# Kernel tuning notes

Hardware: AMD Instinct MI355X
Metric: run time of the kernel (lower is better)

The kernel has to match this reference:

```python
import jax, jax.numpy as jnp
import numpy as np

BITS = 4
N_PACK = 8  # 32-bit container / 4-bit values
GROUPSIZE = 128
MASK = (1 << BITS) - 1


def _unpack(packed, n_valid):
    # packed: [R, ceil(n_valid/N_PACK)] int32 -> [R, n_valid] int32 nibbles
    shifts = (jnp.arange(N_PACK, dtype=jnp.int32) * BITS)
    vals = (packed[:, :, None] >> shifts) & MASK  # [R, C, N_PACK]
    return vals.reshape(packed.shape[0], -1)[:, :n_valid]


def setup_inputs() -> dict:
    key = jax.random.key(0)
    k0, k1, k2, k3, k4 = jax.random.split(key, 5)
    O, I = 4096, 4096
    ng = I // GROUPSIZE  # 32
    x = jax.random.normal(k0, (2, 2048, I), dtype=jnp.float32)
    packed_weight = jax.random.randint(k1, (O, I // N_PACK), 0, 2147483647, dtype=jnp.int32)
    scale = jax.random.uniform(k2, (O, ng), dtype=jnp.float32)
    packed_zp = jax.random.randint(k3, (O, (ng + N_PACK - 1) // N_PACK), 0, 2147483647, dtype=jnp.int32)
    bias = jax.random.normal(k4, (O,), dtype=jnp.float32)
    return {"x": x, "packed_weight": packed_weight, "scale": scale,
            "packed_zp": packed_zp, "bias": bias}


def reference(x, packed_weight, scale, packed_zp, bias):
    O, ng = scale.shape
    I = packed_weight.shape[1] * N_PACK
    # unpack uint4 weights and zero-points (matches torch recover(): shift+mask)
    w_int = _unpack(packed_weight, I)          # [O, I] values in [0, 15]
    zp_int = _unpack(packed_zp, ng)            # [O, ng]
    # per-group dequant: (w - zp) * scale
    w = w_int.reshape(O, ng, GROUPSIZE).astype(scale.dtype)
    fp_weight = ((w - zp_int[:, :, None].astype(scale.dtype)) * scale[:, :, None]).reshape(O, I)
    # F.linear: x @ W^T + b
    return jnp.einsum('bsi,oi->bso', x, fp_weight) + bias
```

## Files before the change

kernel.cpp:

```cpp
#include <hip/hip_runtime.h>
#include <stdint.h>

typedef __attribute__((ext_vector_type(4))) float  floatx4;
typedef __attribute__((ext_vector_type(8))) short  shortx8;
typedef __attribute__((ext_vector_type(4))) unsigned short ushortx4;

typedef unsigned int   u32;
typedef unsigned short u16;

#define TILE    128
#define BK      64
#define THREADS 256
#define CHUNK   (TILE * BK)

__device__ __forceinline__ u32 pack2bf(float f0, float f1) {
    u32 u0 = __builtin_bit_cast(u32, f0) + 0x8000u;
    u32 u1 = __builtin_bit_cast(u32, f1) + 0x8000u;
    return __builtin_amdgcn_perm(u1, u0, 0x07060302u);
}

__device__ __forceinline__ unsigned short f2bf(float f) {
    u32 u = __builtin_bit_cast(u32, f);
    u += 0x7FFFu + ((u >> 16) & 1u);
    return (unsigned short)(u >> 16);
}

__global__ __launch_bounds__(THREADS)
void convert_x(const float* __restrict__ x, u16* __restrict__ At, int I, int KT) {
    const int row  = blockIdx.x;
    const int cseg = blockIdx.y * THREADS + threadIdx.x;
    const int col  = cseg * 8;
    const int mt = row >> 7, r = row & 127;
    const int kt = col >> 6, cs = (col >> 3) & 7;
    const float4 v0 = *(const float4*)(x + (size_t)row * I + col);
    const float4 v1 = *(const float4*)(x + (size_t)row * I + col + 4);
    u32 p[4];
    p[0] = pack2bf(v0.x, v0.y);
    p[1] = pack2bf(v0.z, v0.w);
    p[2] = pack2bf(v1.x, v1.y);
    p[3] = pack2bf(v1.z, v1.w);
    *(uint4*)(At + (size_t)(mt * KT + kt) * CHUNK + r * BK + cs * 8) = *(uint4*)p;
}

__global__ __launch_bounds__(THREADS)
void dequant_w(const int* __restrict__ pw, const float* __restrict__ scale,
               const int* __restrict__ pzp, u16* __restrict__ Bt,
               int I, int ng, int KT) {
    const int o    = blockIdx.x;
    const int wcol = blockIdx.y * THREADS + threadIdx.x;
    const int g  = wcol >> 4;
    const int kt = wcol >> 3, cs = wcol & 7;
    const int nt = o >> 7, r = o & 127;
    const u32 wq = (u32)pw[(size_t)o * (I >> 3) + wcol];
    const float s = scale[o * ng + g];
    const int zpw = pzp[o * ((ng + 7) >> 3) + (g >> 3)];
    const int zp  = (zpw >> ((g & 7) * 4)) & 15;
    const float nzc = -s * (float)(zp + 128);
    float v[8];
    #pragma unroll
    for (int j = 0; j < 8; j++) {
        u32 t;
        if (j < 4)       t = (wq << (16 - 4 * j)) & 0x000F0000u;
        else if (j == 4) t = wq & 0x000F0000u;
        else             t = (wq >> (4 * j - 16)) & 0x000F0000u;
        float f = __builtin_bit_cast(float, t | 0x43000000u);
        v[j] = __builtin_fmaf(f, s, nzc);
    }
    u32 p[4];
    p[0] = pack2bf(v[0], v[1]);
    p[1] = pack2bf(v[2], v[3]);
    p[2] = pack2bf(v[4], v[5]);
    p[3] = pack2bf(v[6], v[7]);
    *(uint4*)(Bt + (size_t)(nt * KT + kt) * CHUNK + r * BK + cs * 8) = *(uint4*)p;
}

__global__ __launch_bounds__(THREADS, 2)
void gemm_bf16(const u16* __restrict__ At, const u16* __restrict__ Bt,
               const float* __restrict__ bias, float* __restrict__ out,
               int O, int KT) {
    __shared__ u16 As[CHUNK];
    __shared__ u16 Bs[CHUNK];

    const int tid = threadIdx.x;
    const int nblk_n = O / TILE;
    const int mt = blockIdx.x / nblk_n;
    const int nt = blockIdx.x % nblk_n;
    const int w = tid >> 6, lane = tid & 63;
    const int wm = w >> 1, wn = w & 1;
    const int l15 = lane & 15, l4 = lane >> 4;

    floatx4 acc[4][4];
    #pragma unroll
    for (int i = 0; i < 4; i++)
        #pragma unroll
        for (int j = 0; j < 4; j++)
            acc[i][j] = (floatx4){0.f, 0.f, 0.f, 0.f};

    for (int kt = 0; kt < KT; kt++) {
        const u16* ga = At + (size_t)(mt * KT + kt) * CHUNK;
        const u16* gb = Bt + (size_t)(nt * KT + kt) * CHUNK;
        __syncthreads();
        #pragma unroll
        for (int it = 0; it < 4; it++) {
            const int off = (it * THREADS + tid) * 8;
            __builtin_amdgcn_global_load_lds((const __attribute__((address_space(1))) u32*)(ga + off),
                                             (__attribute__((address_space(3))) u32*)(As + off),
                                             16, 0, 0);
            __builtin_amdgcn_global_load_lds((const __attribute__((address_space(1))) u32*)(gb + off),
                                             (__attribute__((address_space(3))) u32*)(Bs + off),
                                             16, 0, 0);
        }
        __syncthreads();

        #pragma unroll
        for (int ks = 0; ks < 2; ks++) {
            shortx8 af[4], bf[4];
            #pragma unroll
            for (int i = 0; i < 4; i++)
                af[i] = *(const shortx8*)(&As[(wm * 64 + i * 16 + l15) * BK + ks * 32 + l4 * 8]);
            #pragma unroll
            for (int j = 0; j < 4; j++)
                bf[j] = *(const shortx8*)(&Bs[(wn * 64 + j * 16 + l15) * BK + ks * 32 + l4 * 8]);
            #pragma unroll
            for (int i = 0; i < 4; i++)
                #pragma unroll
                for (int j = 0; j < 4; j++)
                    acc[i][j] = __builtin_amdgcn_mfma_f32_16x16x32_bf16(af[i], bf[j], acc[i][j], 0, 0, 0);
        }
    }

    #pragma unroll
    for (int j = 0; j < 4; j++) {
        int col  = nt * TILE + wn * 64 + j * 16 + l15;
        float bv = bias[col];
        #pragma unroll
        for (int i = 0; i < 4; i++) {
            int rowb = (blockIdx.x / nblk_n) * TILE + wm * 64 + i * 16 + l4 * 4;
            #pragma unroll
            for (int r = 0; r < 4; r++)
                out[(size_t)(rowb + r) * O + col] = acc[i][j][r] + bv;
        }
    }
}

#define LDA 72
__global__ __launch_bounds__(THREADS, 2)
void wql_fused(const float* __restrict__ x, const int* __restrict__ pw,
               const float* __restrict__ scale, const int* __restrict__ pzp,
               const float* __restrict__ bias, float* __restrict__ out,
               int M, int O, int I, int ng)
{
    __shared__ unsigned short As[TILE * LDA];
    __shared__ unsigned short Bs[TILE * LDA];
    const int tid = threadIdx.x;
    const int nblk_n = O / TILE;
    const int mt = blockIdx.x / nblk_n, nt = blockIdx.x % nblk_n;
    const int w = tid >> 6, lane = tid & 63;
    const int wm = w >> 1, wn = w & 1;
    const int l15 = lane & 15, l4 = lane >> 4;
    const int pw_rowlen = I / 8, zp_rowlen = (ng + 7) / 8, GS = I / ng;

    floatx4 acc[4][4];
    #pragma unroll
    for (int i = 0; i < 4; i++)
        #pragma unroll
        for (int j = 0; j < 4; j++) acc[i][j] = (floatx4){0.f, 0.f, 0.f, 0.f};

    const int nk = I / BK;
    for (int kt = 0; kt < nk; kt++) {
        __syncthreads();
        #pragma unroll
        for (int it = 0; it < 8; it++) {
            int f = tid + it * THREADS;
            int row = f >> 4, seg = f & 15;
            const float4 v = *(const float4*)(x + (size_t)(mt * TILE + row) * I + kt * BK + seg * 4);
            ushortx4 b;
            b.x = f2bf(v.x); b.y = f2bf(v.y); b.z = f2bf(v.z); b.w = f2bf(v.w);
            *(ushortx4*)(&As[row * LDA + seg * 4]) = b;
        }
        const int g = (kt * BK) / GS;
        #pragma unroll
        for (int it = 0; it < 4; it++) {
            int e = tid + it * THREADS;
            int row = e >> 3, c = e & 7;
            int o = nt * TILE + row;
            int wq = pw[(size_t)o * pw_rowlen + kt * (BK / 8) + c];
            float s = scale[o * ng + g];
            int zpw = pzp[o * zp_rowlen + (g >> 3)];
            int zp = (zpw >> ((g & 7) * 4)) & 15;
            shortx8 b;
            #pragma unroll
            for (int j = 0; j < 8; j++) {
                int nib = (wq >> (4 * j)) & 15;
                b[j] = (short)f2bf((float)(nib - zp) * s);
            }
            *(shortx8*)(&Bs[row * LDA + c * 8]) = b;
        }
        __syncthreads();
        #pragma unroll
        for (int ks = 0; ks < 2; ks++) {
            shortx8 af[4], bf[4];
            #pragma unroll
            for (int i = 0; i < 4; i++)
                af[i] = *(const shortx8*)(&As[(wm * 64 + i * 16 + l15) * LDA + ks * 32 + l4 * 8]);
            #pragma unroll
            for (int j = 0; j < 4; j++)
                bf[j] = *(const shortx8*)(&Bs[(wn * 64 + j * 16 + l15) * LDA + ks * 32 + l4 * 8]);
            #pragma unroll
            for (int i = 0; i < 4; i++)
                #pragma unroll
                for (int j = 0; j < 4; j++)
                    acc[i][j] = __builtin_amdgcn_mfma_f32_16x16x32_bf16(af[i], bf[j], acc[i][j], 0, 0, 0);
        }
    }
    #pragma unroll
    for (int j = 0; j < 4; j++) {
        int col = nt * TILE + wn * 64 + j * 16 + l15;
        float bv = bias[col];
        #pragma unroll
        for (int i = 0; i < 4; i++) {
            int rowb = mt * TILE + wm * 64 + i * 16 + l4 * 4;
            #pragma unroll
            for (int r = 0; r < 4; r++)
                out[(size_t)(rowb + r) * O + col] = acc[i][j][r] + bv;
        }
    }
}

extern "C" void kernel_launch(void* const* d_in, const int* in_sizes, int n_in,
                              void* d_out, int out_size, void* d_ws, size_t ws_size,
                              hipStream_t stream) {
    const float* x     = (const float*)d_in[0];
    const int*   pw    = (const int*)d_in[1];
    const float* scale = (const float*)d_in[2];
    const int*   pzp   = (const int*)d_in[3];
    const float* bias  = (const float*)d_in[4];
    float*       out   = (float*)d_out;

    const int O  = in_sizes[4];
    const int ng = in_sizes[2] / O;
    const int I  = (in_sizes[1] / O) * 8;
    const int M  = in_sizes[0] / I;
    const int KT = I / BK;

    const size_t need = ((size_t)M * I + (size_t)O * I) * sizeof(u16);
    if (ws_size >= need) {
        u16* At = (u16*)d_ws;
        u16* Bt = At + (size_t)M * I;
        convert_x<<<dim3(M, I / (8 * THREADS)), THREADS, 0, stream>>>(x, At, I, KT);
        dequant_w<<<dim3(O, I / (8 * THREADS)), THREADS, 0, stream>>>(pw, scale, pzp, Bt, I, ng, KT);
        gemm_bf16<<<dim3((M / TILE) * (O / TILE)), THREADS, 0, stream>>>(At, Bt, bias, out, O, KT);
    } else {
        wql_fused<<<dim3((M / TILE) * (O / TILE)), THREADS, 0, stream>>>(x, pw, scale, pzp, bias, out, M, O, I, ng);
    }
}
```

Before: 287.9 us.

## XOR-swizzle LDS tile layout and merge x/weight prep into one kernel

```diff
diff --git a/kernel.cpp b/kernel.cpp
--- a/kernel.cpp
+++ b/kernel.cpp
@@ -26,52 +26,56 @@
 }
 
 __global__ __launch_bounds__(THREADS)
-void convert_x(const float* __restrict__ x, u16* __restrict__ At, int I, int KT) {
-    const int row  = blockIdx.x;
-    const int cseg = blockIdx.y * THREADS + threadIdx.x;
-    const int col  = cseg * 8;
-    const int mt = row >> 7, r = row & 127;
-    const int kt = col >> 6, cs = (col >> 3) & 7;
-    const float4 v0 = *(const float4*)(x + (size_t)row * I + col);
-    const float4 v1 = *(const float4*)(x + (size_t)row * I + col + 4);
-    u32 p[4];
-    p[0] = pack2bf(v0.x, v0.y);
-    p[1] = pack2bf(v0.z, v0.w);
-    p[2] = pack2bf(v1.x, v1.y);
-    p[3] = pack2bf(v1.z, v1.w);
-    *(uint4*)(At + (size_t)(mt * KT + kt) * CHUNK + r * BK + cs * 8) = *(uint4*)p;
-}
-
-__global__ __launch_bounds__(THREADS)
-void dequant_w(const int* __restrict__ pw, const float* __restrict__ scale,
-               const int* __restrict__ pzp, u16* __restrict__ Bt,
-               int I, int ng, int KT) {
-    const int o    = blockIdx.x;
-    const int wcol = blockIdx.y * THREADS + threadIdx.x;
-    const int g  = wcol >> 4;
-    const int kt = wcol >> 3, cs = wcol & 7;
-    const int nt = o >> 7, r = o & 127;
-    const u32 wq = (u32)pw[(size_t)o * (I >> 3) + wcol];
-    const float s = scale[o * ng + g];
-    const int zpw = pzp[o * ((ng + 7) >> 3) + (g >> 3)];
-    const int zp  = (zpw >> ((g & 7) * 4)) & 15;
-    const float nzc = -s * (float)(zp + 128);
-    float v[8];
-    #pragma unroll
-    for (int j = 0; j < 8; j++) {
-        u32 t;
-        if (j < 4)       t = (wq << (16 - 4 * j)) & 0x000F0000u;
-        else if (j == 4) t = wq & 0x000F0000u;
-        else             t = (wq >> (4 * j - 16)) & 0x000F0000u;
-        float f = __builtin_bit_cast(float, t | 0x43000000u);
-        v[j] = __builtin_fmaf(f, s, nzc);
-    }
-    u32 p[4];
-    p[0] = pack2bf(v[0], v[1]);
-    p[1] = pack2bf(v[2], v[3]);
-    p[2] = pack2bf(v[4], v[5]);
-    p[3] = pack2bf(v[6], v[7]);
-    *(uint4*)(Bt + (size_t)(nt * KT + kt) * CHUNK + r * BK + cs * 8) = *(uint4*)p;
+void prep_kernel(const float* __restrict__ x, const int* __restrict__ pw,
+                 const float* __restrict__ scale, const int* __restrict__ pzp,
+                 u16* __restrict__ At, u16* __restrict__ Bt,
+                 int M, int O, int I, int ng, int KT) {
+    const int bid = blockIdx.x;
+    const int t   = threadIdx.x;
+    if (bid < M * 2) {
+        const int row  = bid >> 1;
+        const int cseg = (bid & 1) * THREADS + t;
+        const int kt = cseg >> 3, cp = cseg & 7;
+        const int r = row & (TILE - 1), mt = row >> 7;
+        const int c = cp ^ (r & 7);
+        const float4 v0 = *(const float4*)(x + (size_t)row * I + kt * BK + c * 8);
+        const float4 v1 = *(const float4*)(x + (size_t)row * I + kt * BK + c * 8 + 4);
+        u32 p[4];
+        p[0] = pack2bf(v0.x, v0.y);
+        p[1] = pack2bf(v0.z, v0.w);
+        p[2] = pack2bf(v1.x, v1.y);
+        p[3] = pack2bf(v1.z, v1.w);
+        *(uint4*)(At + (size_t)(mt * KT + kt) * CHUNK + r * BK + cp * 8) = *(uint4*)p;
+    } else {
+        const int bid2 = bid - M * 2;
+        const int o    = bid2 >> 1;
+        const int wpos = (bid2 & 1) * THREADS + t;
+        const int kt = wpos >> 3, cp = wpos & 7;
+        const int r = o & (TILE - 1), nt = o >> 7;
+        const int c = cp ^ (r & 7);
+        const u32 wq = (u32)pw[(size_t)o * (I >> 3) + kt * 8 + c];
+        const int g  = (kt * BK) / (I / ng);
+        const float s = scale[o * ng + g];
+        const int zpw = pzp[o * ((ng + 7) >> 3) + (g >> 3)];
+        const int zp  = (zpw >> ((g & 7) * 4)) & 15;
+        const float nzc = -s * (float)(zp + 128);
+        float v[8];
+        #pragma unroll
+        for (int j = 0; j < 8; j++) {
+            u32 tt;
+            if (j < 4)       tt = (wq << (16 - 4 * j)) & 0x000F0000u;
+            else if (j == 4) tt = wq & 0x000F0000u;
+            else             tt = (wq >> (4 * j - 16)) & 0x000F0000u;
+            float f = __builtin_bit_cast(float, tt | 0x43000000u);
+            v[j] = __builtin_fmaf(f, s, nzc);
+        }
+        u32 p[4];
+        p[0] = pack2bf(v[0], v[1]);
+        p[1] = pack2bf(v[2], v[3]);
+        p[2] = pack2bf(v[4], v[5]);
+        p[3] = pack2bf(v[6], v[7]);
+        *(uint4*)(Bt + (size_t)(nt * KT + kt) * CHUNK + r * BK + cp * 8) = *(uint4*)p;
+    }
 }
 
 __global__ __launch_bounds__(THREADS, 2)
@@ -88,6 +92,7 @@
     const int w = tid >> 6, lane = tid & 63;
     const int wm = w >> 1, wn = w & 1;
     const int l15 = lane & 15, l4 = lane >> 4;
+    const int sw  = l15 & 7;
 
     floatx4 acc[4][4];
     #pragma unroll
@@ -117,10 +122,10 @@
             shortx8 af[4], bf[4];
             #pragma unroll
             for (int i = 0; i < 4; i++)
-                af[i] = *(const shortx8*)(&As[(wm * 64 + i * 16 + l15) * BK + ks * 32 + l4 * 8]);
+                af[i] = *(const shortx8*)(&As[(wm * 64 + i * 16 + l15) * BK + ((ks * 4 + l4) ^ sw) * 8]);
             #pragma unroll
             for (int j = 0; j < 4; j++)
-                bf[j] = *(const shortx8*)(&Bs[(wn * 64 + j * 16 + l15) * BK + ks * 32 + l4 * 8]);
+                bf[j] = *(const shortx8*)(&Bs[(wn * 64 + j * 16 + l15) * BK + ((ks * 4 + l4) ^ sw) * 8]);
             #pragma unroll
             for (int i = 0; i < 4; i++)
                 #pragma unroll
@@ -135,7 +140,7 @@
         float bv = bias[col];
         #pragma unroll
         for (int i = 0; i < 4; i++) {
-            int rowb = (blockIdx.x / nblk_n) * TILE + wm * 64 + i * 16 + l4 * 4;
+            int rowb = mt * TILE + wm * 64 + i * 16 + l4 * 4;
             #pragma unroll
             for (int r = 0; r < 4; r++)
                 out[(size_t)(rowb + r) * O + col] = acc[i][j][r] + bv;
@@ -247,8 +252,7 @@
     if (ws_size >= need) {
         u16* At = (u16*)d_ws;
         u16* Bt = At + (size_t)M * I;
-        convert_x<<<dim3(M, I / (8 * THREADS)), THREADS, 0, stream>>>(x, At, I, KT);
-        dequant_w<<<dim3(O, I / (8 * THREADS)), THREADS, 0, stream>>>(pw, scale, pzp, Bt, I, ng, KT);
+        prep_kernel<<<dim3(M * 2 + O * 2), THREADS, 0, stream>>>(x, pw, scale, pzp, At, Bt, M, O, I, ng, KT);
         gemm_bf16<<<dim3((M / TILE) * (O / TILE)), THREADS, 0, stream>>>(At, Bt, bias, out, O, KT);
     } else {
         wql_fused<<<dim3((M / TILE) * (O / TILE)), THREADS, 0, stream>>>(x, pw, scale, pzp, bias, out, M, O, I, ng);
```

Measured after the change: 257.6 us. 10.5% less time.
